# Kernel optimization log

Hardware: AMD Instinct MI355X
Metric: run time of the kernel (lower is better)

Reference implementation:

```python
import jax, jax.numpy as jnp
import numpy as np

B, NSV, NTRK, K, H = 512, 128, 512, 8, 16


def setup_inputs() -> dict:
    key = jax.random.key(0)
    ks = jax.random.split(key, 12)
    p = lambda k, shp: (jax.random.normal(k, shp, dtype=jnp.float32) * 0.1)
    return {
        "x_sv": jax.random.normal(ks[0], (B * NSV, 2), dtype=jnp.float32),
        "x_trk": jax.random.normal(ks[1], (B * NTRK, 8), dtype=jnp.float32),
        "batch_sv": jnp.repeat(jnp.arange(B, dtype=jnp.int32), NSV),
        "batch_trk": jnp.repeat(jnp.arange(B, dtype=jnp.int32), NTRK),
        # sv_encode: Linear(2,16) -> ELU -> Linear(16,16)
        "W1s": p(ks[2], (2, H)), "b1s": jnp.zeros((H,), jnp.float32),
        "W2s": p(ks[3], (H, H)), "b2s": jnp.zeros((H,), jnp.float32),
        # trk_encode: Linear(8,16) -> ELU -> Linear(16,16)
        "W1t": p(ks[4], (8, H)), "b1t": jnp.zeros((H,), jnp.float32),
        "W2t": p(ks[5], (H, H)), "b2t": jnp.zeros((H,), jnp.float32),
        # edge MLP: Linear(2*16, 16)
        "We": p(ks[6], (2 * H, H)), "be": jnp.zeros((H,), jnp.float32),
        # output head: Linear(16, 1)
        "Wo": p(ks[7], (H, 1)), "bo": jnp.zeros((1,), jnp.float32),
    }


def reference(x_sv, x_trk, batch_sv, batch_trk,
              W1s, b1s, W2s, b2s, W1t, b1t, W2t, b2t, We, be, Wo, bo):
    # Node encoders
    sv = jax.nn.elu(x_sv @ W1s + b1s) @ W2s + b2s      # [Nsv, H]
    trk = jax.nn.elu(x_trk @ W1t + b1t) @ W2t + b2t    # [Ntrk, H]

    # Regular batching: reshape to per-event blocks (batch_sv/batch_trk are
    # contiguous repeats of arange(B) with NSV / NTRK nodes per event).
    svb = sv.reshape(B, NSV, H)      # [B, S, H]
    trkb = trk.reshape(B, NTRK, H)   # [B, T, H]

    # kNN in encoded space: squared L2 distance per event, k nearest SVs per track
    t_sq = jnp.sum(trkb * trkb, -1)[:, :, None]          # [B, T, 1]
    s_sq = jnp.sum(svb * svb, -1)[:, None, :]            # [B, 1, S]
    dots = jnp.einsum("bth,bsh->bts", trkb, svb)         # [B, T, S]
    d2 = t_sq + s_sq - 2.0 * dots                        # [B, T, S]
    _, idx = jax.lax.top_k(-d2, K)                       # [B, T, K] indices into S

    # Gather neighbor SV features: [B, T, K, H]
    nbr = jax.vmap(lambda s, i: s[i])(svb, idx)

    # EdgeConv message: nn(cat[x_i, x_j - x_i]), x_i = track (target), x_j = SV
    ti = trkb[:, :, None, :]                                    # [B, T, 1, H]
    msg_in = jnp.concatenate(
        [jnp.broadcast_to(ti, nbr.shape), nbr - ti], axis=-1)   # [B, T, K, 2H]
    msg = msg_in @ We + be                                      # [B, T, K, H]
    feats = jnp.max(msg, axis=2).reshape(B * NTRK, H)           # max aggregation

    # Output head + per-event average pool (avg_pool_x with cluster == batch)
    out = jax.nn.sigmoid(feats @ Wo + bo)                       # [Ntrk, 1]
    sums = jax.ops.segment_sum(out, batch_trk, num_segments=B)  # [B, 1]
    cnts = jax.ops.segment_sum(jnp.ones_like(out), batch_trk, num_segments=B)
    pooled = sums / cnts                                        # [B, 1]
    batch_out = jnp.arange(B, dtype=jnp.int32)
    return pooled, batch_out
```

## Files before the change

kernel.cpp:

```cpp
#include <hip/hip_runtime.h>
#include <cmath>

#define BB   512
#define NSV  128
#define NTRK 512
#define KK   8
#define HH   16
#define TPB  512
#define PSTR 20

__device__ __forceinline__ float elu_f(float x) {
    return x > 0.0f ? x : expm1f(x);
}
__device__ __forceinline__ unsigned umin_u(unsigned a, unsigned b) { return a < b ? a : b; }
__device__ __forceinline__ unsigned med3u(unsigned a, unsigned b, unsigned c) {
    unsigned d;
    asm("v_med3_u32 %0, %1, %2, %3" : "=v"(d) : "v"(a), "v"(b), "v"(c));
    return d;
}

__global__ __launch_bounds__(NSV) void precompute(
    const float* __restrict__ x_sv,
    const float* __restrict__ W1s, const float* __restrict__ b1s,
    const float* __restrict__ W2s, const float* __restrict__ b2s,
    const float* __restrict__ We,  const float* __restrict__ be,
    const float* __restrict__ Wo,  const float* __restrict__ bo,
    float* __restrict__ svf_g, float* __restrict__ proj_g,
    float* __restrict__ hsq_g, float* __restrict__ uc_g)
{
    const int b = blockIdx.x, s = threadIdx.x;

    const float* xp = x_sv + (size_t)(b * NSV + s) * 2;
    float x0 = xp[0], x1 = xp[1];
    float hb[HH];
    #pragma unroll
    for (int h = 0; h < HH; ++h)
        hb[h] = elu_f(x0 * W1s[h] + x1 * W1s[HH + h] + b1s[h]);

    float o[HH];
    float sq = 0.0f;
    #pragma unroll
    for (int h2 = 0; h2 < HH; ++h2) {
        float a = b2s[h2];
        #pragma unroll
        for (int h = 0; h < HH; ++h) a += hb[h] * W2s[h * HH + h2];
        o[h2] = a;
        sq += a * a;
    }

    float* sdst = svf_g + (size_t)(b * NSV + s) * HH;
    #pragma unroll
    for (int h4 = 0; h4 < 4; ++h4)
        *(float4*)&sdst[h4 * 4] = make_float4(o[h4*4], o[h4*4+1], o[h4*4+2], o[h4*4+3]);
    hsq_g[b * NSV + s] = 0.5f * sq;

    float* pdst = proj_g + (size_t)(b * NSV + s) * HH;
    #pragma unroll
    for (int h4 = 0; h4 < 4; ++h4) {
        float p[4];
        #pragma unroll
        for (int q = 0; q < 4; ++q) {
            int h = h4 * 4 + q;
            float a = 0.0f;
            #pragma unroll
            for (int j = 0; j < HH; ++j) a += o[j] * We[(HH + j) * HH + h];
            p[q] = a;
        }
        *(float4*)&pdst[h4 * 4] = make_float4(p[0], p[1], p[2], p[3]);
    }

    if (b == 0) {
        if (s < HH) {
            float a = 0.0f;
            #pragma unroll
            for (int h = 0; h < HH; ++h)
                a += (We[s * HH + h] - We[(HH + s) * HH + h]) * Wo[h];
            uc_g[s] = a;
        } else if (s == HH) {
            float a = bo[0];
            #pragma unroll
            for (int h = 0; h < HH; ++h) a += be[h] * Wo[h];
            uc_g[HH] = a;
        }
    }
}

__global__ __launch_bounds__(TPB, 4) void fused_main(
    const float* __restrict__ x_trk,
    const float* __restrict__ W1t, const float* __restrict__ b1t,
    const float* __restrict__ W2t, const float* __restrict__ b2t,
    const float* __restrict__ Wo,
    const float* __restrict__ svf_g, const float* __restrict__ proj_g,
    const float* __restrict__ hsq_g, const float* __restrict__ uc_g,
    float* __restrict__ out)
{
    __shared__ float proj[NSV][PSTR];
    __shared__ float sred[TPB / 64];

    const int b = blockIdx.x, tid = threadIdx.x;

    {
        int s = tid >> 2, q = tid & 3;
        float4 p = *(const float4*)&proj_g[(size_t)(b * NSV + s) * HH + q * 4];
        *(float4*)&proj[s][q * 4] = p;
    }

    float tf[HH], ntf[HH], htsq;
    {
        const float* xp = x_trk + (size_t)(b * NTRK + tid) * 8;
        float x[8];
        *(float4*)&x[0] = *(const float4*)&xp[0];
        *(float4*)&x[4] = *(const float4*)&xp[4];
        float hb[HH];
        #pragma unroll
        for (int h = 0; h < HH; ++h) {
            float a = b1t[h];
            #pragma unroll
            for (int i = 0; i < 8; ++i) a += x[i] * W1t[i * HH + h];
            hb[h] = elu_f(a);
        }
        float sq = 0.0f;
        #pragma unroll
        for (int h2 = 0; h2 < HH; ++h2) {
            float a = b2t[h2];
            #pragma unroll
            for (int h = 0; h < HH; ++h) a += hb[h] * W2t[h * HH + h2];
            tf[h2] = a;
            ntf[h2] = -a;
            sq += a * a;
        }
        htsq = 0.5f * sq;
    }

    unsigned k[KK];
    #pragma unroll
    for (int q = 0; q < KK; ++q) k[q] = 0xFFFFFFFFu;

    __syncthreads();

    const float* __restrict__ svb = svf_g + (size_t)b * NSV * HH;
    const float* __restrict__ hsb = hsq_g + (size_t)b * NSV;

    float pa[HH], pb[HH], ha, hbv;

    #define LOADROW(buf, hv, idx)                         \
        do {                                              \
            const float* _sp = svb + (idx) * HH;          \
            _Pragma("unroll")                             \
            for (int _j = 0; _j < HH; ++_j) buf[_j] = _sp[_j]; \
            hv = hsb[idx];                                \
        } while (0)

    #define BODY(buf, hv, idx)                                        \
        do {                                                          \
            float a0 = fmaf(ntf[0], buf[0], htsq);                    \
            float a1 = fmaf(ntf[1], buf[1], hv);                      \
            float a2 = ntf[2] * buf[2];                               \
            float a3 = ntf[3] * buf[3];                               \
            _Pragma("unroll")                                         \
            for (int _j = 4; _j < HH; _j += 4) {                      \
                a0 = fmaf(ntf[_j],     buf[_j],     a0);              \
                a1 = fmaf(ntf[_j + 1], buf[_j + 1], a1);              \
                a2 = fmaf(ntf[_j + 2], buf[_j + 2], a2);              \
                a3 = fmaf(ntf[_j + 3], buf[_j + 3], a3);              \
            }                                                         \
            float e = fmaxf((a0 + a1) + (a2 + a3), 0.0f);             \
            unsigned v = (__float_as_uint(e) & 0xFFFFFF80u) | (unsigned)(idx); \
            unsigned nk0 = umin_u(v, k[0]);                           \
            unsigned nk1 = med3u(v, k[0], k[1]);                      \
            unsigned nk2 = med3u(v, k[1], k[2]);                      \
            unsigned nk3 = med3u(v, k[2], k[3]);                      \
            unsigned nk4 = med3u(v, k[3], k[4]);                      \
            unsigned nk5 = med3u(v, k[4], k[5]);                      \
            unsigned nk6 = med3u(v, k[5], k[6]);                      \
            unsigned nk7 = med3u(v, k[6], k[7]);                      \
            k[0] = nk0; k[1] = nk1; k[2] = nk2; k[3] = nk3;           \
            k[4] = nk4; k[5] = nk5; k[6] = nk6; k[7] = nk7;           \
        } while (0)

    LOADROW(pa, ha, 0);
    LOADROW(pb, hbv, 1);
    for (int s = 0; s < NSV - 2; s += 2) {
        BODY(pa, ha, s);
        LOADROW(pa, ha, s + 2);
        BODY(pb, hbv, s + 1);
        LOADROW(pb, hbv, s + 3);
    }
    BODY(pa, ha, NSV - 2);
    BODY(pb, hbv, NSV - 1);

    #undef LOADROW
    #undef BODY

    float local;
    {
        float acc = uc_g[HH];
        #pragma unroll
        for (int j = 0; j < HH; ++j) acc = fmaf(tf[j], uc_g[j], acc);

        float mx[HH];
        #pragma unroll
        for (int h = 0; h < HH; ++h) mx[h] = -INFINITY;
        #pragma unroll
        for (int q = 0; q < KK; ++q) {
            const float* pr = &proj[k[q] & 127u][0];
            #pragma unroll
            for (int h4 = 0; h4 < 4; ++h4) {
                float4 p = *(const float4*)&pr[h4 * 4];
                mx[h4 * 4 + 0] = fmaxf(mx[h4 * 4 + 0], p.x);
                mx[h4 * 4 + 1] = fmaxf(mx[h4 * 4 + 1], p.y);
                mx[h4 * 4 + 2] = fmaxf(mx[h4 * 4 + 2], p.z);
                mx[h4 * 4 + 3] = fmaxf(mx[h4 * 4 + 3], p.w);
            }
        }
        #pragma unroll
        for (int h = 0; h < HH; ++h) acc = fmaf(mx[h], Wo[h], acc);
        local = 1.0f / (1.0f + expf(-acc));
    }

    #pragma unroll
    for (int off = 32; off > 0; off >>= 1)
        local += __shfl_down(local, off, 64);
    if ((tid & 63) == 0) sred[tid >> 6] = local;
    __syncthreads();
    if (tid == 0) {
        float tot = 0.0f;
        #pragma unroll
        for (int w = 0; w < TPB / 64; ++w) tot += sred[w];
        out[b]      = tot * (1.0f / NTRK);
        out[BB + b] = (float)b;
    }
}

extern "C" void kernel_launch(void* const* d_in, const int* in_sizes, int n_in,
                              void* d_out, int out_size, void* d_ws, size_t ws_size,
                              hipStream_t stream) {
    const float* x_sv  = (const float*)d_in[0];
    const float* x_trk = (const float*)d_in[1];
    const float* W1s = (const float*)d_in[4];
    const float* b1s = (const float*)d_in[5];
    const float* W2s = (const float*)d_in[6];
    const float* b2s = (const float*)d_in[7];
    const float* W1t = (const float*)d_in[8];
    const float* b1t = (const float*)d_in[9];
    const float* W2t = (const float*)d_in[10];
    const float* b2t = (const float*)d_in[11];
    const float* We  = (const float*)d_in[12];
    const float* be  = (const float*)d_in[13];
    const float* Wo  = (const float*)d_in[14];
    const float* bo  = (const float*)d_in[15];
    float* out = (float*)d_out;

    float* svf_g  = (float*)d_ws;
    float* proj_g = svf_g  + (size_t)BB * NSV * HH;
    float* hsq_g  = proj_g + (size_t)BB * NSV * HH;
    float* uc_g   = hsq_g  + (size_t)BB * NSV;

    precompute<<<BB, NSV, 0, stream>>>(x_sv, W1s, b1s, W2s, b2s, We, be, Wo, bo,
                                       svf_g, proj_g, hsq_g, uc_g);
    fused_main<<<BB, TPB, 0, stream>>>(x_trk, W1t, b1t, W2t, b2t, Wo,
                                       svf_g, proj_g, hsq_g, uc_g, out);
}
```

Measured before the change: 132.7 us.

## Split SV scan across two threads per track and quarter events across blocks

Each event is now handled by four blocks of 256 threads, each block covering 128 tracks. Two threads share each track and scan half of the 128 SVs each. Their partial top-8 lists are merged through shared memory with an elementwise min against the reversed partner list. The per-event mean is combined across the four blocks with atomics and a last-block counter, and the pool and counter buffers are zeroed in the precompute kernel. This halves the serial kNN scan per thread and raises block count and occupancy, at the cost of running the track encoder twice per track and adding cross-block atomics.

```diff
diff --git a/kernel.cpp b/kernel.cpp
--- a/kernel.cpp
+++ b/kernel.cpp
@@ -6,8 +6,9 @@
 #define NTRK 512
 #define KK   8
 #define HH   16
-#define TPB  512
+#define TPB  256
 #define PSTR 20
+#define KSTR 17
 
 __device__ __forceinline__ float elu_f(float x) {
     return x > 0.0f ? x : expm1f(x);
@@ -26,9 +27,12 @@
     const float* __restrict__ We,  const float* __restrict__ be,
     const float* __restrict__ Wo,  const float* __restrict__ bo,
     float* __restrict__ svf_g, float* __restrict__ proj_g,
-    float* __restrict__ hsq_g, float* __restrict__ uc_g)
+    float* __restrict__ hsq_g, float* __restrict__ uc_g,
+    float* __restrict__ pool_g, unsigned* __restrict__ cnt_g)
 {
     const int b = blockIdx.x, s = threadIdx.x;
+
+    if (s == 0) { pool_g[b] = 0.0f; cnt_g[b] = 0u; }
 
     const float* xp = x_sv + (size_t)(b * NSV + s) * 2;
     float x0 = xp[0], x1 = xp[1];
@@ -85,29 +89,38 @@
     }
 }
 
-__global__ __launch_bounds__(TPB, 4) void fused_main(
+__global__ __launch_bounds__(TPB, 8) void fused_main(
     const float* __restrict__ x_trk,
     const float* __restrict__ W1t, const float* __restrict__ b1t,
     const float* __restrict__ W2t, const float* __restrict__ b2t,
     const float* __restrict__ Wo,
     const float* __restrict__ svf_g, const float* __restrict__ proj_g,
     const float* __restrict__ hsq_g, const float* __restrict__ uc_g,
+    float* __restrict__ pool_g, unsigned* __restrict__ cnt_g,
     float* __restrict__ out)
 {
-    __shared__ float proj[NSV][PSTR];
-    __shared__ float sred[TPB / 64];
-
-    const int b = blockIdx.x, tid = threadIdx.x;
-
-    {
-        int s = tid >> 2, q = tid & 3;
-        float4 p = *(const float4*)&proj_g[(size_t)(b * NSV + s) * HH + q * 4];
-        *(float4*)&proj[s][q * 4] = p;
+    __shared__ float    proj[NSV][PSTR];
+    __shared__ unsigned kbuf[NSV][KSTR];
+    __shared__ float    sred[TPB / 64];
+
+    const int blk = blockIdx.x;
+    const int b   = blk >> 2, qtr = blk & 3;
+    const int tid = threadIdx.x;
+    const int tl  = tid & 127;
+    const int trk = qtr * 128 + tl;
+    const int sh  = __builtin_amdgcn_readfirstlane(tid >> 7);
+
+    float4 stv[2]; int ss[2], sq4[2];
+    #pragma unroll
+    for (int r = 0; r < 2; ++r) {
+        int e = tid + r * TPB;
+        ss[r] = e >> 2; sq4[r] = e & 3;
+        stv[r] = *(const float4*)&proj_g[(size_t)(b * NSV + ss[r]) * HH + sq4[r] * 4];
     }
 
     float tf[HH], ntf[HH], htsq;
     {
-        const float* xp = x_trk + (size_t)(b * NTRK + tid) * 8;
+        const float* xp = x_trk + (size_t)(b * NTRK + trk) * 8;
         float x[8];
         *(float4*)&x[0] = *(const float4*)&xp[0];
         *(float4*)&x[4] = *(const float4*)&xp[4];
@@ -136,19 +149,18 @@
     #pragma unroll
     for (int q = 0; q < KK; ++q) k[q] = 0xFFFFFFFFu;
 
-    __syncthreads();
-
-    const float* __restrict__ svb = svf_g + (size_t)b * NSV * HH;
-    const float* __restrict__ hsb = hsq_g + (size_t)b * NSV;
+    const int sbase = sh * 64;
+    const float* __restrict__ svb = svf_g + (size_t)(b * NSV + sbase) * HH;
+    const float* __restrict__ hsb = hsq_g + (size_t)b * NSV + sbase;
 
     float pa[HH], pb[HH], ha, hbv;
 
-    #define LOADROW(buf, hv, idx)                         \
-        do {                                              \
-            const float* _sp = svb + (idx) * HH;          \
-            _Pragma("unroll")                             \
-            for (int _j = 0; _j < HH; ++_j) buf[_j] = _sp[_j]; \
-            hv = hsb[idx];                                \
+    #define LOADROW(buf, hv, idx)                                \
+        do {                                                     \
+            const float* _sp = svb + (idx) * HH;                 \
+            _Pragma("unroll")                                    \
+            for (int _j = 0; _j < HH; ++_j) buf[_j] = _sp[_j];   \
+            hv = hsb[idx];                                       \
         } while (0)
 
     #define BODY(buf, hv, idx)                                        \
@@ -165,7 +177,8 @@
                 a3 = fmaf(ntf[_j + 3], buf[_j + 3], a3);              \
             }                                                         \
             float e = fmaxf((a0 + a1) + (a2 + a3), 0.0f);             \
-            unsigned v = (__float_as_uint(e) & 0xFFFFFF80u) | (unsigned)(idx); \
+            unsigned v = (__float_as_uint(e) & 0xFFFFFF80u)           \
+                         | (unsigned)(sbase + (idx));                 \
             unsigned nk0 = umin_u(v, k[0]);                           \
             unsigned nk1 = med3u(v, k[0], k[1]);                      \
             unsigned nk2 = med3u(v, k[1], k[2]);                      \
@@ -180,17 +193,31 @@
 
     LOADROW(pa, ha, 0);
     LOADROW(pb, hbv, 1);
-    for (int s = 0; s < NSV - 2; s += 2) {
+    for (int s = 0; s < 64 - 2; s += 2) {
         BODY(pa, ha, s);
         LOADROW(pa, ha, s + 2);
         BODY(pb, hbv, s + 1);
         LOADROW(pb, hbv, s + 3);
     }
-    BODY(pa, ha, NSV - 2);
-    BODY(pb, hbv, NSV - 1);
+    BODY(pa, ha, 62);
+    BODY(pb, hbv, 63);
 
     #undef LOADROW
     #undef BODY
+
+    #pragma unroll
+    for (int q = 0; q < KK; ++q) kbuf[tl][sh * 8 + q] = k[q];
+    #pragma unroll
+    for (int r = 0; r < 2; ++r)
+        *(float4*)&proj[ss[r]][sq4[r] * 4] = stv[r];
+    __syncthreads();
+
+    unsigned m[KK];
+    {
+        const unsigned* pk = &kbuf[tl][(sh ^ 1) * 8];
+        #pragma unroll
+        for (int i = 0; i < KK; ++i) m[i] = umin_u(k[i], pk[7 - i]);
+    }
 
     float local;
     {
@@ -203,7 +230,7 @@
         for (int h = 0; h < HH; ++h) mx[h] = -INFINITY;
         #pragma unroll
         for (int q = 0; q < KK; ++q) {
-            const float* pr = &proj[k[q] & 127u][0];
+            const float* pr = &proj[m[q] & 127u][0];
             #pragma unroll
             for (int h4 = 0; h4 < 4; ++h4) {
                 float4 p = *(const float4*)&pr[h4 * 4];
@@ -224,11 +251,15 @@
     if ((tid & 63) == 0) sred[tid >> 6] = local;
     __syncthreads();
     if (tid == 0) {
-        float tot = 0.0f;
-        #pragma unroll
-        for (int w = 0; w < TPB / 64; ++w) tot += sred[w];
-        out[b]      = tot * (1.0f / NTRK);
-        out[BB + b] = (float)b;
+        float part = sred[0] + sred[1] + sred[2] + sred[3];
+        atomicAdd(&pool_g[b], part);
+        __threadfence();
+        unsigned old = atomicAdd(&cnt_g[b], 1u);
+        if (old == 3u) {
+            float tot = atomicAdd(&pool_g[b], 0.0f);
+            out[b]      = tot * (1.0f / (2 * NTRK));
+            out[BB + b] = (float)b;
+        }
     }
 }
 
@@ -251,13 +282,16 @@
     const float* bo  = (const float*)d_in[15];
     float* out = (float*)d_out;
 
-    float* svf_g  = (float*)d_ws;
-    float* proj_g = svf_g  + (size_t)BB * NSV * HH;
-    float* hsq_g  = proj_g + (size_t)BB * NSV * HH;
-    float* uc_g   = hsq_g  + (size_t)BB * NSV;
+    float*    svf_g  = (float*)d_ws;
+    float*    proj_g = svf_g  + (size_t)BB * NSV * HH;
+    float*    hsq_g  = proj_g + (size_t)BB * NSV * HH;
+    float*    uc_g   = hsq_g  + (size_t)BB * NSV;
+    float*    pool_g = uc_g   + 32;
+    unsigned* cnt_g  = (unsigned*)(pool_g + BB);
 
     precompute<<<BB, NSV, 0, stream>>>(x_sv, W1s, b1s, W2s, b2s, We, be, Wo, bo,
-                                       svf_g, proj_g, hsq_g, uc_g);
-    fused_main<<<BB, TPB, 0, stream>>>(x_trk, W1t, b1t, W2t, b2t, Wo,
-                                       svf_g, proj_g, hsq_g, uc_g, out);
-}
+                                       svf_g, proj_g, hsq_g, uc_g, pool_g, cnt_g);
+    fused_main<<<BB * 4, TPB, 0, stream>>>(x_trk, W1t, b1t, W2t, b2t, Wo,
+                                           svf_g, proj_g, hsq_g, uc_g,
+                                           pool_g, cnt_g, out);
+}
```

Result: slower. 179.6 us (+35.3%).

## Pack SV half-norm into padded rows and hand-pipeline scalar loads with inline asm

Applied to the files above, without the earlier changes.

The SV feature rows are padded to 20 floats with the half squared norm stored in slot 16, so one row is fetched with four dwordx4 loads plus one dword. The kNN scan becomes a 4-deep software pipeline of inline-asm global loads with explicit s_waitcnt vmcnt(15), so memory latency overlaps the distance and top-k work. The row pointer is an SGPR, which makes these wave-uniform loads. This also removes the separate hsq buffer and the negated-feature register array. The risks are that inline asm hides the loads from the compiler's scheduler, and that the final iteration issues loads past the end of the event's rows.

```diff
diff --git a/kernel.cpp b/kernel.cpp
--- a/kernel.cpp
+++ b/kernel.cpp
@@ -7,7 +7,10 @@
 #define KK   8
 #define HH   16
 #define TPB  512
+#define RSTR 20
 #define PSTR 20
+
+typedef float vf4 __attribute__((ext_vector_type(4)));
 
 __device__ __forceinline__ float elu_f(float x) {
     return x > 0.0f ? x : expm1f(x);
@@ -26,7 +29,7 @@
     const float* __restrict__ We,  const float* __restrict__ be,
     const float* __restrict__ Wo,  const float* __restrict__ bo,
     float* __restrict__ svf_g, float* __restrict__ proj_g,
-    float* __restrict__ hsq_g, float* __restrict__ uc_g)
+    float* __restrict__ uc_g)
 {
     const int b = blockIdx.x, s = threadIdx.x;
 
@@ -48,11 +51,11 @@
         sq += a * a;
     }
 
-    float* sdst = svf_g + (size_t)(b * NSV + s) * HH;
+    float* sdst = svf_g + (size_t)(b * NSV + s) * RSTR;
     #pragma unroll
     for (int h4 = 0; h4 < 4; ++h4)
         *(float4*)&sdst[h4 * 4] = make_float4(o[h4*4], o[h4*4+1], o[h4*4+2], o[h4*4+3]);
-    hsq_g[b * NSV + s] = 0.5f * sq;
+    sdst[HH] = 0.5f * sq;
 
     float* pdst = proj_g + (size_t)(b * NSV + s) * HH;
     #pragma unroll
@@ -91,7 +94,7 @@
     const float* __restrict__ W2t, const float* __restrict__ b2t,
     const float* __restrict__ Wo,
     const float* __restrict__ svf_g, const float* __restrict__ proj_g,
-    const float* __restrict__ hsq_g, const float* __restrict__ uc_g,
+    const float* __restrict__ uc_g,
     float* __restrict__ out)
 {
     __shared__ float proj[NSV][PSTR];
@@ -105,7 +108,7 @@
         *(float4*)&proj[s][q * 4] = p;
     }
 
-    float tf[HH], ntf[HH], htsq;
+    float tf[HH], htsq;
     {
         const float* xp = x_trk + (size_t)(b * NTRK + tid) * 8;
         float x[8];
@@ -126,7 +129,6 @@
             #pragma unroll
             for (int h = 0; h < HH; ++h) a += hb[h] * W2t[h * HH + h2];
             tf[h2] = a;
-            ntf[h2] = -a;
             sq += a * a;
         }
         htsq = 0.5f * sq;
@@ -138,58 +140,75 @@
 
     __syncthreads();
 
-    const float* __restrict__ svb = svf_g + (size_t)b * NSV * HH;
-    const float* __restrict__ hsb = hsq_g + (size_t)b * NSV;
-
-    float pa[HH], pb[HH], ha, hbv;
-
-    #define LOADROW(buf, hv, idx)                         \
-        do {                                              \
-            const float* _sp = svb + (idx) * HH;          \
-            _Pragma("unroll")                             \
-            for (int _j = 0; _j < HH; ++_j) buf[_j] = _sp[_j]; \
-            hv = hsb[idx];                                \
+    const float* ip = svf_g + (size_t)b * NSV * RSTR;
+    unsigned vzero = 0;
+
+    vf4 q00, q01, q02, q03; float h0;
+    vf4 q10, q11, q12, q13; float h1;
+    vf4 q20, q21, q22, q23; float h2;
+    vf4 q30, q31, q32, q33; float h3;
+
+    #define ISSUE_ROW(R)                                                   \
+        do {                                                               \
+            asm volatile(                                                  \
+                "global_load_dwordx4 %0, %5, %6 offset:0\n\t"              \
+                "global_load_dwordx4 %1, %5, %6 offset:16\n\t"             \
+                "global_load_dwordx4 %2, %5, %6 offset:32\n\t"             \
+                "global_load_dwordx4 %3, %5, %6 offset:48\n\t"             \
+                "global_load_dword %4, %5, %6 offset:64"                   \
+                : "=v"(q##R##0), "=v"(q##R##1), "=v"(q##R##2),             \
+                  "=v"(q##R##3), "=v"(h##R)                                \
+                : "v"(vzero), "s"(ip));                                    \
+            ip += RSTR;                                                    \
         } while (0)
 
-    #define BODY(buf, hv, idx)                                        \
-        do {                                                          \
-            float a0 = fmaf(ntf[0], buf[0], htsq);                    \
-            float a1 = fmaf(ntf[1], buf[1], hv);                      \
-            float a2 = ntf[2] * buf[2];                               \
-            float a3 = ntf[3] * buf[3];                               \
-            _Pragma("unroll")                                         \
-            for (int _j = 4; _j < HH; _j += 4) {                      \
-                a0 = fmaf(ntf[_j],     buf[_j],     a0);              \
-                a1 = fmaf(ntf[_j + 1], buf[_j + 1], a1);              \
-                a2 = fmaf(ntf[_j + 2], buf[_j + 2], a2);              \
-                a3 = fmaf(ntf[_j + 3], buf[_j + 3], a3);              \
-            }                                                         \
-            float e = fmaxf((a0 + a1) + (a2 + a3), 0.0f);             \
-            unsigned v = (__float_as_uint(e) & 0xFFFFFF80u) | (unsigned)(idx); \
-            unsigned nk0 = umin_u(v, k[0]);                           \
-            unsigned nk1 = med3u(v, k[0], k[1]);                      \
-            unsigned nk2 = med3u(v, k[1], k[2]);                      \
-            unsigned nk3 = med3u(v, k[2], k[3]);                      \
-            unsigned nk4 = med3u(v, k[3], k[4]);                      \
-            unsigned nk5 = med3u(v, k[4], k[5]);                      \
-            unsigned nk6 = med3u(v, k[5], k[6]);                      \
-            unsigned nk7 = med3u(v, k[6], k[7]);                      \
-            k[0] = nk0; k[1] = nk1; k[2] = nk2; k[3] = nk3;           \
-            k[4] = nk4; k[5] = nk5; k[6] = nk6; k[7] = nk7;           \
+    #define WAIT_ROW(R)                                                    \
+        asm volatile("s_waitcnt vmcnt(15)"                                 \
+                     : "+v"(q##R##0), "+v"(q##R##1), "+v"(q##R##2),        \
+                       "+v"(q##R##3), "+v"(h##R))
+
+    #define BODY(a, bq, c, d, hv, idx)                                     \
+        do {                                                               \
+            float a0 = fmaf(-tf[0], a[0], htsq);                           \
+            float a1 = fmaf(-tf[1], a[1], hv);                             \
+            float a2 = -tf[2] * a[2];                                      \
+            float a3 = -tf[3] * a[3];                                      \
+            a0 = fmaf(-tf[4],  bq[0], a0); a1 = fmaf(-tf[5],  bq[1], a1);  \
+            a2 = fmaf(-tf[6],  bq[2], a2); a3 = fmaf(-tf[7],  bq[3], a3);  \
+            a0 = fmaf(-tf[8],  c[0],  a0); a1 = fmaf(-tf[9],  c[1],  a1);  \
+            a2 = fmaf(-tf[10], c[2],  a2); a3 = fmaf(-tf[11], c[3],  a3);  \
+            a0 = fmaf(-tf[12], d[0],  a0); a1 = fmaf(-tf[13], d[1],  a1);  \
+            a2 = fmaf(-tf[14], d[2],  a2); a3 = fmaf(-tf[15], d[3],  a3);  \
+            float e = fmaxf((a0 + a1) + (a2 + a3), 0.0f);                  \
+            unsigned v = (__float_as_uint(e) & 0xFFFFFF80u)                \
+                         | (unsigned)(idx);                                \
+            unsigned nk0 = umin_u(v, k[0]);                                \
+            unsigned nk1 = med3u(v, k[0], k[1]);                           \
+            unsigned nk2 = med3u(v, k[1], k[2]);                           \
+            unsigned nk3 = med3u(v, k[2], k[3]);                           \
+            unsigned nk4 = med3u(v, k[3], k[4]);                           \
+            unsigned nk5 = med3u(v, k[4], k[5]);                           \
+            unsigned nk6 = med3u(v, k[5], k[6]);                           \
+            unsigned nk7 = med3u(v, k[6], k[7]);                           \
+            k[0] = nk0; k[1] = nk1; k[2] = nk2; k[3] = nk3;                \
+            k[4] = nk4; k[5] = nk5; k[6] = nk6; k[7] = nk7;                \
         } while (0)
 
-    LOADROW(pa, ha, 0);
-    LOADROW(pb, hbv, 1);
-    for (int s = 0; s < NSV - 2; s += 2) {
-        BODY(pa, ha, s);
-        LOADROW(pa, ha, s + 2);
-        BODY(pb, hbv, s + 1);
-        LOADROW(pb, hbv, s + 3);
-    }
-    BODY(pa, ha, NSV - 2);
-    BODY(pb, hbv, NSV - 1);
-
-    #undef LOADROW
+    ISSUE_ROW(0); ISSUE_ROW(1); ISSUE_ROW(2); ISSUE_ROW(3);
+    for (int s = 0; s < NSV; s += 4) {
+        WAIT_ROW(0); BODY(q00, q01, q02, q03, h0, s + 0); ISSUE_ROW(0);
+        WAIT_ROW(1); BODY(q10, q11, q12, q13, h1, s + 1); ISSUE_ROW(1);
+        WAIT_ROW(2); BODY(q20, q21, q22, q23, h2, s + 2); ISSUE_ROW(2);
+        WAIT_ROW(3); BODY(q30, q31, q32, q33, h3, s + 3); ISSUE_ROW(3);
+    }
+    asm volatile("s_waitcnt vmcnt(0)"
+                 : "+v"(q00), "+v"(q01), "+v"(q02), "+v"(q03), "+v"(h0),
+                   "+v"(q10), "+v"(q11), "+v"(q12), "+v"(q13), "+v"(h1),
+                   "+v"(q20), "+v"(q21), "+v"(q22), "+v"(q23), "+v"(h2),
+                   "+v"(q30), "+v"(q31), "+v"(q32), "+v"(q33), "+v"(h3));
+
+    #undef ISSUE_ROW
+    #undef WAIT_ROW
     #undef BODY
 
     float local;
@@ -252,12 +271,11 @@
     float* out = (float*)d_out;
 
     float* svf_g  = (float*)d_ws;
-    float* proj_g = svf_g  + (size_t)BB * NSV * HH;
-    float* hsq_g  = proj_g + (size_t)BB * NSV * HH;
-    float* uc_g   = hsq_g  + (size_t)BB * NSV;
+    float* proj_g = svf_g  + (size_t)BB * NSV * RSTR;
+    float* uc_g   = proj_g + (size_t)BB * NSV * HH;
 
     precompute<<<BB, NSV, 0, stream>>>(x_sv, W1s, b1s, W2s, b2s, We, be, Wo, bo,
-                                       svf_g, proj_g, hsq_g, uc_g);
+                                       svf_g, proj_g, uc_g);
     fused_main<<<BB, TPB, 0, stream>>>(x_trk, W1t, b1t, W2t, b2t, Wo,
-                                       svf_g, proj_g, hsq_g, uc_g, out);
-}
+                                       svf_g, proj_g, uc_g, out);
+}
```

New measurement: 169.0 us. 1.27x slower.

## Fuse SV precompute into main kernel and use packed fp32 distance math

Applied to the files above, without the earlier changes.

Merges the SV encoder and projection precompute into the main per-event kernel. Projections and the head constants now go straight to shared memory, and the SV features plus half squared norm are written as one padded global row that the same block reads back after the barrier. The distance dot product is rewritten with two-wide float vectors so the compiler can emit packed FMA, which aims to remove one launch, the proj/uc global round trip and half the dot-product instructions. The risk is that the write and read buffers alias despite restrict qualifiers, and the kernel relies on block-level visibility of global writes after __syncthreads.

```diff
diff --git a/kernel.cpp b/kernel.cpp
--- a/kernel.cpp
+++ b/kernel.cpp
@@ -7,7 +7,10 @@
 #define KK   8
 #define HH   16
 #define TPB  512
+#define RSTR 20
 #define PSTR 20
+
+typedef float vf2 __attribute__((ext_vector_type(2)));
 
 __device__ __forceinline__ float elu_f(float x) {
     return x > 0.0f ? x : expm1f(x);
@@ -19,93 +22,68 @@
     return d;
 }
 
-__global__ __launch_bounds__(NSV) void precompute(
-    const float* __restrict__ x_sv,
+__global__ __launch_bounds__(TPB, 4) void fused_all(
+    const float* __restrict__ x_sv, const float* __restrict__ x_trk,
     const float* __restrict__ W1s, const float* __restrict__ b1s,
     const float* __restrict__ W2s, const float* __restrict__ b2s,
+    const float* __restrict__ W1t, const float* __restrict__ b1t,
+    const float* __restrict__ W2t, const float* __restrict__ b2t,
     const float* __restrict__ We,  const float* __restrict__ be,
     const float* __restrict__ Wo,  const float* __restrict__ bo,
-    float* __restrict__ svf_g, float* __restrict__ proj_g,
-    float* __restrict__ hsq_g, float* __restrict__ uc_g)
-{
-    const int b = blockIdx.x, s = threadIdx.x;
-
-    const float* xp = x_sv + (size_t)(b * NSV + s) * 2;
-    float x0 = xp[0], x1 = xp[1];
-    float hb[HH];
-    #pragma unroll
-    for (int h = 0; h < HH; ++h)
-        hb[h] = elu_f(x0 * W1s[h] + x1 * W1s[HH + h] + b1s[h]);
-
-    float o[HH];
-    float sq = 0.0f;
-    #pragma unroll
-    for (int h2 = 0; h2 < HH; ++h2) {
-        float a = b2s[h2];
-        #pragma unroll
-        for (int h = 0; h < HH; ++h) a += hb[h] * W2s[h * HH + h2];
-        o[h2] = a;
-        sq += a * a;
-    }
-
-    float* sdst = svf_g + (size_t)(b * NSV + s) * HH;
-    #pragma unroll
-    for (int h4 = 0; h4 < 4; ++h4)
-        *(float4*)&sdst[h4 * 4] = make_float4(o[h4*4], o[h4*4+1], o[h4*4+2], o[h4*4+3]);
-    hsq_g[b * NSV + s] = 0.5f * sq;
-
-    float* pdst = proj_g + (size_t)(b * NSV + s) * HH;
-    #pragma unroll
-    for (int h4 = 0; h4 < 4; ++h4) {
-        float p[4];
-        #pragma unroll
-        for (int q = 0; q < 4; ++q) {
-            int h = h4 * 4 + q;
-            float a = 0.0f;
-            #pragma unroll
-            for (int j = 0; j < HH; ++j) a += o[j] * We[(HH + j) * HH + h];
-            p[q] = a;
-        }
-        *(float4*)&pdst[h4 * 4] = make_float4(p[0], p[1], p[2], p[3]);
-    }
-
-    if (b == 0) {
-        if (s < HH) {
-            float a = 0.0f;
-            #pragma unroll
-            for (int h = 0; h < HH; ++h)
-                a += (We[s * HH + h] - We[(HH + s) * HH + h]) * Wo[h];
-            uc_g[s] = a;
-        } else if (s == HH) {
-            float a = bo[0];
-            #pragma unroll
-            for (int h = 0; h < HH; ++h) a += be[h] * Wo[h];
-            uc_g[HH] = a;
-        }
-    }
-}
-
-__global__ __launch_bounds__(TPB, 4) void fused_main(
-    const float* __restrict__ x_trk,
-    const float* __restrict__ W1t, const float* __restrict__ b1t,
-    const float* __restrict__ W2t, const float* __restrict__ b2t,
-    const float* __restrict__ Wo,
-    const float* __restrict__ svf_g, const float* __restrict__ proj_g,
-    const float* __restrict__ hsq_g, const float* __restrict__ uc_g,
+    float* __restrict__ svw,
+    const float* __restrict__ svr,
     float* __restrict__ out)
 {
     __shared__ float proj[NSV][PSTR];
+    __shared__ float ucS[HH + 1];
     __shared__ float sred[TPB / 64];
 
     const int b = blockIdx.x, tid = threadIdx.x;
 
-    {
-        int s = tid >> 2, q = tid & 3;
-        float4 p = *(const float4*)&proj_g[(size_t)(b * NSV + s) * HH + q * 4];
-        *(float4*)&proj[s][q * 4] = p;
-    }
-
-    float tf[HH], ntf[HH], htsq;
+    if (tid < NSV) {
+        const float* xp = x_sv + (size_t)(b * NSV + tid) * 2;
+        float x0 = xp[0], x1 = xp[1];
+        float hb[HH];
+        #pragma unroll
+        for (int h = 0; h < HH; ++h)
+            hb[h] = elu_f(x0 * W1s[h] + x1 * W1s[HH + h] + b1s[h]);
+        float o[HH], sq = 0.0f;
+        #pragma unroll
+        for (int h2 = 0; h2 < HH; ++h2) {
+            float a = b2s[h2];
+            #pragma unroll
+            for (int h = 0; h < HH; ++h) a += hb[h] * W2s[h * HH + h2];
+            o[h2] = a;
+            sq += a * a;
+        }
+        float* dst = svw + (size_t)(b * NSV + tid) * RSTR;
+        #pragma unroll
+        for (int h4 = 0; h4 < 4; ++h4)
+            *(float4*)&dst[h4 * 4] = make_float4(o[h4*4], o[h4*4+1], o[h4*4+2], o[h4*4+3]);
+        dst[HH] = 0.5f * sq;
+        #pragma unroll
+        for (int h = 0; h < HH; ++h) {
+            float a = 0.0f;
+            #pragma unroll
+            for (int j = 0; j < HH; ++j) a += o[j] * We[(HH + j) * HH + h];
+            proj[tid][h] = a;
+        }
+    } else if (tid < NSV + HH) {
+        int j = tid - NSV;
+        float a = 0.0f;
+        #pragma unroll
+        for (int h = 0; h < HH; ++h)
+            a += (We[j * HH + h] - We[(HH + j) * HH + h]) * Wo[h];
+        ucS[j] = a;
+    } else if (tid == NSV + HH) {
+        float a = bo[0];
+        #pragma unroll
+        for (int h = 0; h < HH; ++h) a += be[h] * Wo[h];
+        ucS[HH] = a;
+    }
+
+    float tf[HH], htsq;
+    vf2 ntfp[8];
     {
         const float* xp = x_trk + (size_t)(b * NTRK + tid) * 8;
         float x[8];
@@ -126,10 +104,14 @@
             #pragma unroll
             for (int h = 0; h < HH; ++h) a += hb[h] * W2t[h * HH + h2];
             tf[h2] = a;
-            ntf[h2] = -a;
             sq += a * a;
         }
         htsq = 0.5f * sq;
+        #pragma unroll
+        for (int j = 0; j < 8; ++j) {
+            vf2 t; t.x = -tf[2 * j]; t.y = -tf[2 * j + 1];
+            ntfp[j] = t;
+        }
     }
 
     unsigned k[KK];
@@ -138,44 +120,43 @@
 
     __syncthreads();
 
-    const float* __restrict__ svb = svf_g + (size_t)b * NSV * HH;
-    const float* __restrict__ hsb = hsq_g + (size_t)b * NSV;
-
-    float pa[HH], pb[HH], ha, hbv;
-
-    #define LOADROW(buf, hv, idx)                         \
-        do {                                              \
-            const float* _sp = svb + (idx) * HH;          \
-            _Pragma("unroll")                             \
-            for (int _j = 0; _j < HH; ++_j) buf[_j] = _sp[_j]; \
-            hv = hsb[idx];                                \
+    const float* rp = svr + (size_t)b * NSV * RSTR;
+
+    vf2 pa[8], pb[8]; float ha, hbv;
+
+    #define LOADROW(buf, hv, idx)                                      \
+        do {                                                           \
+            const float* _r = rp + (size_t)(idx) * RSTR;               \
+            _Pragma("unroll")                                          \
+            for (int _j = 0; _j < 8; ++_j)                             \
+                buf[_j] = *(const vf2*)(_r + 2 * _j);                  \
+            hv = _r[HH];                                               \
         } while (0)
 
-    #define BODY(buf, hv, idx)                                        \
-        do {                                                          \
-            float a0 = fmaf(ntf[0], buf[0], htsq);                    \
-            float a1 = fmaf(ntf[1], buf[1], hv);                      \
-            float a2 = ntf[2] * buf[2];                               \
-            float a3 = ntf[3] * buf[3];                               \
-            _Pragma("unroll")                                         \
-            for (int _j = 4; _j < HH; _j += 4) {                      \
-                a0 = fmaf(ntf[_j],     buf[_j],     a0);              \
-                a1 = fmaf(ntf[_j + 1], buf[_j + 1], a1);              \
-                a2 = fmaf(ntf[_j + 2], buf[_j + 2], a2);              \
-                a3 = fmaf(ntf[_j + 3], buf[_j + 3], a3);              \
-            }                                                         \
-            float e = fmaxf((a0 + a1) + (a2 + a3), 0.0f);             \
-            unsigned v = (__float_as_uint(e) & 0xFFFFFF80u) | (unsigned)(idx); \
-            unsigned nk0 = umin_u(v, k[0]);                           \
-            unsigned nk1 = med3u(v, k[0], k[1]);                      \
-            unsigned nk2 = med3u(v, k[1], k[2]);                      \
-            unsigned nk3 = med3u(v, k[2], k[3]);                      \
-            unsigned nk4 = med3u(v, k[3], k[4]);                      \
-            unsigned nk5 = med3u(v, k[4], k[5]);                      \
-            unsigned nk6 = med3u(v, k[5], k[6]);                      \
-            unsigned nk7 = med3u(v, k[6], k[7]);                      \
-            k[0] = nk0; k[1] = nk1; k[2] = nk2; k[3] = nk3;           \
-            k[4] = nk4; k[5] = nk5; k[6] = nk6; k[7] = nk7;           \
+    #define BODY(buf, hv, idx)                                         \
+        do {                                                           \
+            vf2 a0 = ntfp[0] * buf[0];                                 \
+            vf2 a1 = ntfp[1] * buf[1];                                 \
+            vf2 a2 = ntfp[2] * buf[2];                                 \
+            vf2 a3 = ntfp[3] * buf[3];                                 \
+            a0 = __builtin_elementwise_fma(ntfp[4], buf[4], a0);       \
+            a1 = __builtin_elementwise_fma(ntfp[5], buf[5], a1);       \
+            a2 = __builtin_elementwise_fma(ntfp[6], buf[6], a2);       \
+            a3 = __builtin_elementwise_fma(ntfp[7], buf[7], a3);       \
+            a0 = a0 + a1; a2 = a2 + a3; a0 = a0 + a2;                  \
+            float e = fmaxf((htsq + hv) + (a0.x + a0.y), 0.0f);        \
+            unsigned v = (__float_as_uint(e) & 0xFFFFFF80u)            \
+                         | (unsigned)(idx);                            \
+            unsigned nk0 = umin_u(v, k[0]);                            \
+            unsigned nk1 = med3u(v, k[0], k[1]);                       \
+            unsigned nk2 = med3u(v, k[1], k[2]);                       \
+            unsigned nk3 = med3u(v, k[2], k[3]);                       \
+            unsigned nk4 = med3u(v, k[3], k[4]);                       \
+            unsigned nk5 = med3u(v, k[4], k[5]);                       \
+            unsigned nk6 = med3u(v, k[5], k[6]);                       \
+            unsigned nk7 = med3u(v, k[6], k[7]);                       \
+            k[0] = nk0; k[1] = nk1; k[2] = nk2; k[3] = nk3;            \
+            k[4] = nk4; k[5] = nk5; k[6] = nk6; k[7] = nk7;            \
         } while (0)
 
     LOADROW(pa, ha, 0);
@@ -194,9 +175,9 @@
 
     float local;
     {
-        float acc = uc_g[HH];
-        #pragma unroll
-        for (int j = 0; j < HH; ++j) acc = fmaf(tf[j], uc_g[j], acc);
+        float acc = ucS[HH];
+        #pragma unroll
+        for (int j = 0; j < HH; ++j) acc = fmaf(tf[j], ucS[j], acc);
 
         float mx[HH];
         #pragma unroll
@@ -251,13 +232,11 @@
     const float* bo  = (const float*)d_in[15];
     float* out = (float*)d_out;
 
-    float* svf_g  = (float*)d_ws;
-    float* proj_g = svf_g  + (size_t)BB * NSV * HH;
-    float* hsq_g  = proj_g + (size_t)BB * NSV * HH;
-    float* uc_g   = hsq_g  + (size_t)BB * NSV;
-
-    precompute<<<BB, NSV, 0, stream>>>(x_sv, W1s, b1s, W2s, b2s, We, be, Wo, bo,
-                                       svf_g, proj_g, hsq_g, uc_g);
-    fused_main<<<BB, TPB, 0, stream>>>(x_trk, W1t, b1t, W2t, b2t, Wo,
-                                       svf_g, proj_g, hsq_g, uc_g, out);
-}
+    float* rows = (float*)d_ws;
+
+    fused_all<<<BB, TPB, 0, stream>>>(x_sv, x_trk,
+                                      W1s, b1s, W2s, b2s,
+                                      W1t, b1t, W2t, b2t,
+                                      We, be, Wo, bo,
+                                      rows, rows, out);
+}
```

Result: faster. 125.3 us (-5.6%).
